# Kernel optimization log

Hardware: AMD Instinct MI355X
Metric: run time of the kernel (lower is better)

The kernel has to match this reference:

```python
import jax, jax.numpy as jnp
import numpy as np

ANCHOR_SIZES = (128.0, 256.0, 512.0)
ANCHOR_RATIOS = (0.5, 1.0, 2.0)
IOU_THR = 0.3


def _conv(x, w, b, pad):
    y = jax.lax.conv_general_dilated(
        x, w, window_strides=(1, 1), padding=[(pad, pad), (pad, pad)],
        dimension_numbers=("NCHW", "OIHW", "NCHW"))
    return y + b[None, :, None, None]


def _make_anchors(grid_h, grid_w, stride):
    # torchvision-style cell anchors (ratio-major over scales), rounded
    scales = jnp.asarray(ANCHOR_SIZES, jnp.float32)
    ratios = jnp.asarray(ANCHOR_RATIOS, jnp.float32)
    h_r = jnp.sqrt(ratios)
    w_r = 1.0 / h_r
    ws = (w_r[:, None] * scales[None, :]).reshape(-1)  # (A,)
    hs = (h_r[:, None] * scales[None, :]).reshape(-1)
    base = jnp.round(jnp.stack([-ws, -hs, ws, hs], axis=1) / 2.0)  # (A,4)
    sx = jnp.arange(grid_w, dtype=jnp.float32) * stride
    sy = jnp.arange(grid_h, dtype=jnp.float32) * stride
    yy, xx = jnp.meshgrid(sy, sx, indexing="ij")
    shifts = jnp.stack([xx, yy, xx, yy], axis=-1).reshape(-1, 4)  # (HW,4)
    return (shifts[:, None, :] + base[None, :, :]).reshape(-1, 4)  # (HW*A,4)


def _apply_box(anchors, deltas):
    w = anchors[:, 2] - anchors[:, 0]
    h = anchors[:, 3] - anchors[:, 1]
    cx = anchors[:, 0] + 0.5 * w
    cy = anchors[:, 1] + 0.5 * h
    pcx = deltas[:, 0] * w + cx
    pcy = deltas[:, 1] * h + cy
    pw = jnp.exp(deltas[:, 2]) * w
    ph = jnp.exp(deltas[:, 3]) * h
    return jnp.stack([pcx - 0.5 * pw, pcy - 0.5 * ph,
                      pcx + 0.5 * pw, pcy + 0.5 * ph], axis=1)


def _clip(boxes, img_h, img_w):
    x1 = jnp.clip(boxes[:, 0], 0.0, img_w)
    y1 = jnp.clip(boxes[:, 1], 0.0, img_h)
    x2 = jnp.clip(boxes[:, 2], 0.0, img_w)
    y2 = jnp.clip(boxes[:, 3], 0.0, img_h)
    return jnp.stack([x1, y1, x2, y2], axis=1)


def _nms_keep(boxes, scores, thr):
    # returns boolean keep mask in ORIGINAL box order (all idxs identical in
    # the source's batched_nms call, so this is plain NMS)
    n = boxes.shape[0]
    order = jnp.argsort(-scores)
    b = boxes[order]
    area = (b[:, 2] - b[:, 0]) * (b[:, 3] - b[:, 1])
    lt = jnp.maximum(b[:, None, :2], b[None, :, :2])
    rb = jnp.minimum(b[:, None, 2:], b[None, :, 2:])
    wh = jnp.clip(rb - lt, 0.0, None)
    inter = wh[..., 0] * wh[..., 1]
    iou = inter / (area[:, None] + area[None, :] - inter + 1e-9)  # (N,N)
    idx = jnp.arange(n)

    def body(i, keep):
        sup = (iou[i] > thr) & (idx > i)
        return jnp.where(keep[i], keep & ~sup, keep)

    keep_sorted = jax.lax.fori_loop(0, n, body, jnp.ones(n, bool))
    return jnp.zeros(n, bool).at[order].set(keep_sorted)


def setup_inputs() -> dict:
    key = jax.random.key(0)
    ks = jax.random.split(key, 7)
    C, H, W = 256, 32, 32
    A = len(ANCHOR_SIZES) * len(ANCHOR_RATIOS)  # 9
    return {
        "features": jax.random.normal(ks[0], (1, C, H, W), jnp.float32),
        "image_size": 512,
        "conv_w": jax.random.normal(ks[1], (512, C, 3, 3), jnp.float32) * 0.01,
        "conv_b": jnp.zeros((512,), jnp.float32),
        "cls_w": jax.random.normal(ks[2], (2 * A, 512, 1, 1), jnp.float32) * 0.01,
        "cls_b": jnp.zeros((2 * A,), jnp.float32),
        "bbox_w": jax.random.normal(ks[3], (4 * A, 512, 1, 1), jnp.float32) * 0.01,
        "bbox_b": jnp.zeros((4 * A,), jnp.float32),
    }


def reference(features, image_size, conv_w, conv_b, cls_w, cls_b, bbox_w, bbox_b):
    img_h = img_w = float(image_size)
    x = jax.nn.relu(_conv(features, conv_w, conv_b, pad=1))
    logits = _conv(x, cls_w, cls_b, pad=0)          # (1, 2A, H, W)
    bbox_pred = _conv(x, bbox_w, bbox_b, pad=0)     # (1, 4A, H, W)
    probs = jax.nn.sigmoid(logits)
    fg_scores = probs[:, 1::2, :, :].reshape(-1)    # same flatten order as torch
    grid_h, grid_w = features.shape[2], features.shape[3]
    stride = image_size // grid_h
    anchors = _make_anchors(grid_h, grid_w, float(stride))
    proposals = _apply_box(anchors, bbox_pred.reshape(-1, 4))
    proposals = _clip(proposals, img_h, img_w)
    keep = _nms_keep(proposals, fg_scores, IOU_THR)
    # fixed-shape output: suppressed boxes zeroed, plus the keep mask
    return proposals * keep[:, None].astype(proposals.dtype), probs, keep
```

## Files before the change

kernel.cpp:

```cpp
#include <hip/hip_runtime.h>
#include <math.h>

#define X_B      0
#define BBOX_B   2097152
#define PROPS_B  2244608
#define KEYS_B   2392064
#define RANK_B   2465792
#define SKEYS_B  2502656
#define SBOX_B   2576384
#define MASK_B   2725888
#define WS_NEED  13400000

typedef unsigned long long u64;
typedef double v4d __attribute__((ext_vector_type(4)));

__global__ __launch_bounds__(256, 2) void conv3x3_mfma_k(
    const float* __restrict__ feat, const float* __restrict__ w,
    const float* __restrict__ bias, float* __restrict__ xout)
{
  __shared__ float wl[9280];
  __shared__ float fl[8768];

  const int tid = threadIdx.x;
  const int bid = blockIdx.x;
  const int ct = ((bid & 7) << 2) | ((bid >> 3) >> 4);
  const int g  = (bid >> 3) & 15;
  const int co0 = ct << 4;
  const int y0  = g << 1;

  for (int i = tid; i < 8768; i += 256) fl[i] = 0.0f;

  const int lane = tid & 63, wv = tid >> 6;
  const int q = lane >> 4, n = lane & 15;
  const int wy = wv >> 1, xb = (wv & 1) << 4;
  const int xn = xb + n;

  v4d ac0 = {0.0, 0.0, 0.0, 0.0}, ac1 = {0.0, 0.0, 0.0, 0.0};
  v4d ac2 = {0.0, 0.0, 0.0, 0.0}, ac3 = {0.0, 0.0, 0.0, 0.0};
  const float4* feat4 = (const float4*)feat;

  __syncthreads();

  for (int c = 0; c < 4; ++c) {
    const int cb = c << 6;
    #pragma unroll
    for (int i = 0; i < 9; ++i) {
      const int idx4 = tid + (i << 8);
      const int co = idx4 / 144;
      const int s4 = idx4 - co * 144;
      *(float4*)&wl[co * 580 + (s4 << 2)] =
          *(const float4*)(w + (co0 + co) * 2304 + c * 576 + (s4 << 2));
    }
    #pragma unroll
    for (int i = 0; i < 8; ++i) {
      const int idx4 = tid + (i << 8);
      const int ci = idx4 >> 5;
      const int rr = (idx4 >> 3) & 3;
      const int x4 = idx4 & 7;
      const int grow = y0 - 1 + rr;
      if ((unsigned)grow < 32u) {
        const float4 v = feat4[((cb + ci) << 8) + (grow << 3) + x4];
        float* p = &fl[ci * 137 + rr * 34 + 1 + (x4 << 2)];
        p[0] = v.x; p[1] = v.y; p[2] = v.z; p[3] = v.w;
      }
    }
    __syncthreads();
    #pragma unroll
    for (int tap = 0; tap < 9; ++tap) {
      const int ky = tap / 3, kx = tap - 3 * (tap / 3);
      const float* ab = &wl[n * 580 + q * 9 + tap];
      const float* bb = &fl[q * 137 + (wy + ky) * 34 + xn + kx];
      #pragma unroll
      for (int u = 0; u < 16; u += 4) {
        ac0 = __builtin_amdgcn_mfma_f64_16x16x4f64(
            (double)ab[(u + 0) * 36], (double)bb[(u + 0) * 548], ac0, 0, 0, 0);
        ac1 = __builtin_amdgcn_mfma_f64_16x16x4f64(
            (double)ab[(u + 1) * 36], (double)bb[(u + 1) * 548], ac1, 0, 0, 0);
        ac2 = __builtin_amdgcn_mfma_f64_16x16x4f64(
            (double)ab[(u + 2) * 36], (double)bb[(u + 2) * 548], ac2, 0, 0, 0);
        ac3 = __builtin_amdgcn_mfma_f64_16x16x4f64(
            (double)ab[(u + 3) * 36], (double)bb[(u + 3) * 548], ac3, 0, 0, 0);
      }
    }
    __syncthreads();
  }

  const int pbase = (g << 6) + (wv << 4) + n;
  #pragma unroll
  for (int i = 0; i < 4; ++i) {
    const int co = co0 + q + (i << 2);
    const double s = (ac0[i] + ac1[i]) + (ac2[i] + ac3[i]);
    const double v = fmax(s + (double)bias[co], 0.0);
    xout[(co << 10) + pbase] = (float)v;
  }
}

#define CPITCH 38
#define CCHS   (18 * CPITCH)
__global__ __launch_bounds__(256) void conv3x3_relu_fb_k(
    const float* __restrict__ feat, const float* __restrict__ w,
    const float* __restrict__ bias, float* __restrict__ xout)
{
  __shared__ float il[2][8 * CCHS];
  const int cp = blockIdx.x >> 1, h = blockIdx.x & 1;
  const int tid = threadIdx.x;
  const int h16 = h << 4;
  const int co0 = cp << 1;
  for (int i = tid; i < 8 * CCHS; i += 256) { il[0][i] = 0.0f; il[1][i] = 0.0f; }
  const int yl = tid >> 4;
  const int x0 = (tid & 15) << 1;
  double aA0 = 0.0, aA1 = 0.0, aB0 = 0.0, aB1 = 0.0;
  const float4* feat4 = (const float4*)feat;
  float4 pf[5]; int pch[5], pt[5], pc4[5], pok[5];
  #pragma unroll
  for (int k = 0; k < 5; ++k) {
    const int i = tid + (k << 8);
    const int ch = i / 144, rem = i - ch * 144;
    const int t = rem >> 3, c4 = rem & 7;
    const int g = h16 - 1 + t;
    pch[k] = ch; pt[k] = t; pc4[k] = c4;
    pok[k] = (i < 1152) && ((unsigned)g < 32u);
    pf[k] = pok[k] ? feat4[(ch << 8) + (g << 3) + c4] : float4{0.f,0.f,0.f,0.f};
  }
  __syncthreads();
  for (int cc = 0; cc < 256; cc += 8) {
    const int buf = (cc >> 3) & 1;
    #pragma unroll
    for (int k = 0; k < 5; ++k)
      if (pok[k]) {
        float* p = &il[buf][pch[k] * CCHS + pt[k] * CPITCH + (pc4[k] << 2) + 1];
        p[0] = pf[k].x; p[1] = pf[k].y; p[2] = pf[k].z; p[3] = pf[k].w;
      }
    if (cc + 8 < 256) {
      #pragma unroll
      for (int k = 0; k < 5; ++k) {
        const int g = h16 - 1 + pt[k];
        if (pok[k]) pf[k] = feat4[((cc + 8 + pch[k]) << 8) + (g << 3) + pc4[k]];
      }
    }
    __syncthreads();
    #pragma unroll
    for (int cl = 0; cl < 8; ++cl) {
      const float* wAp = w + co0 * 2304 + (cc + cl) * 9;
      const float* wBp = wAp + 2304;
      double wa[9], wb[9];
      #pragma unroll
      for (int q = 0; q < 9; ++q) { wa[q] = (double)wAp[q]; wb[q] = (double)wBp[q]; }
      const float* ir = &il[buf][cl * CCHS + yl * CPITCH + x0];
      #pragma unroll
      for (int ky = 0; ky < 3; ++ky) {
        const float2 q0 = *(const float2*)(ir + ky * CPITCH);
        const float2 q1 = *(const float2*)(ir + ky * CPITCH + 2);
        const double v0 = (double)q0.x, v1 = (double)q0.y;
        const double v2 = (double)q1.x, v3 = (double)q1.y;
        aA0 += v0 * wa[3*ky+0] + v1 * wa[3*ky+1] + v2 * wa[3*ky+2];
        aA1 += v1 * wa[3*ky+0] + v2 * wa[3*ky+1] + v3 * wa[3*ky+2];
        aB0 += v0 * wb[3*ky+0] + v1 * wb[3*ky+1] + v2 * wb[3*ky+2];
        aB1 += v1 * wb[3*ky+0] + v2 * wb[3*ky+1] + v3 * wb[3*ky+2];
      }
    }
  }
  const double bA = (double)bias[co0], bB = (double)bias[co0 + 1];
  const int y = h16 + yl;
  float2 rA, rB;
  rA.x = (float)fmax(aA0 + bA, 0.0); rA.y = (float)fmax(aA1 + bA, 0.0);
  rB.x = (float)fmax(aB0 + bB, 0.0); rB.y = (float)fmax(aB1 + bB, 0.0);
  *(float2*)&xout[(co0 << 10) + (y << 5) + x0] = rA;
  *(float2*)&xout[((co0 + 1) << 10) + (y << 5) + x0] = rB;
}

__global__ __launch_bounds__(256) void head1x1_k(
    const float* __restrict__ x,
    const float* __restrict__ cls_w, const float* __restrict__ cls_b,
    const float* __restrict__ bbox_w, const float* __restrict__ bbox_b,
    float* __restrict__ out, float* __restrict__ bbox_out)
{
  __shared__ float wl[512];
  const int bid = blockIdx.x;
  const int co = bid >> 2;
  const int px = ((bid & 3) << 8) | threadIdx.x;
  const bool is_cls = co < 18;
  const float* wsrc = is_cls ? (cls_w + co * 512) : (bbox_w + (co - 18) * 512);
  for (int i = threadIdx.x; i < 512; i += 256) wl[i] = wsrc[i];
  __syncthreads();
  double acc0 = 0.0, acc1 = 0.0, acc2 = 0.0, acc3 = 0.0;
  #pragma unroll 4
  for (int c = 0; c < 512; c += 4) {
    acc0 += (double)x[((c + 0) << 10) | px] * (double)wl[c + 0];
    acc1 += (double)x[((c + 1) << 10) | px] * (double)wl[c + 1];
    acc2 += (double)x[((c + 2) << 10) | px] * (double)wl[c + 2];
    acc3 += (double)x[((c + 3) << 10) | px] * (double)wl[c + 3];
  }
  double acc = ((acc0 + acc1) + (acc2 + acc3)) +
               (double)(is_cls ? cls_b[co] : bbox_b[co - 18]);
  if (is_cls)
    out[36864 + (co << 10) + px] = (float)(1.0 / (1.0 + exp(-acc)));
  else
    bbox_out[((co - 18) << 10) + px] = (float)acc;
}

__global__ __launch_bounds__(256) void proposals_k(
    const float* __restrict__ bbox, const int* __restrict__ imgsz,
    const float* __restrict__ out, float* __restrict__ props,
    u64* __restrict__ keys, unsigned* __restrict__ rank)
{
  const int r = blockIdx.x * 256 + threadIdx.x;
  if (r >= 9216) return;
  const float4 d = ((const float4*)bbox)[r];
  const int cell = r / 9, a = r - cell * 9;
  const int ix = cell & 31, iy = cell >> 5;
  const int ri = a / 3, si = a - ri * 3;
  const double ratio = (ri == 0) ? 0.5 : (ri == 1 ? 1.0 : 2.0);
  const double scale = (si == 0) ? 128.0 : (si == 1 ? 256.0 : 512.0);
  const double hr = sqrt(ratio), wr = 1.0 / hr;
  const double bx = nearbyint(wr * scale * 0.5);
  const double by = nearbyint(hr * scale * 0.5);
  const double cx = ix * 16.0, cy = iy * 16.0;
  const double w = 2.0 * bx, hh = 2.0 * by;
  const double pcx = (double)d.x * w + cx;
  const double pcy = (double)d.y * hh + cy;
  const double pw = exp((double)d.z) * w;
  const double ph = exp((double)d.w) * hh;
  const double im = (double)imgsz[0];
  float4 o;
  o.x = (float)fmin(fmax(pcx - 0.5 * pw, 0.0), im);
  o.y = (float)fmin(fmax(pcy - 0.5 * ph, 0.0), im);
  o.z = (float)fmin(fmax(pcx + 0.5 * pw, 0.0), im);
  o.w = (float)fmin(fmax(pcy + 0.5 * ph, 0.0), im);
  ((float4*)props)[r] = o;
  const float s = out[36864 + ((2 * (r >> 10) + 1) << 10) + (r & 1023)];
  keys[r] = ((u64)__float_as_uint(s) << 32) | (unsigned)(0x7FFFFFFF - r);
  rank[r] = 0u;
}

__global__ __launch_bounds__(256) void rank_k(
    const u64* __restrict__ keys, unsigned* __restrict__ rank)
{
  const int jt = blockIdx.x % 36, ic = blockIdx.x / 36;
  const int j = jt * 256 + threadIdx.x;
  const u64 kj = keys[j];
  const int lane = threadIdx.x & 63;
  const int base = ic * 576;
  unsigned lo[9], hi[9];
  #pragma unroll
  for (int rr = 0; rr < 9; ++rr) {
    const u64 k = keys[base + rr * 64 + lane];
    lo[rr] = (unsigned)k; hi[rr] = (unsigned)(k >> 32);
  }
  unsigned cnt = 0;
  #pragma unroll
  for (int rr = 0; rr < 9; ++rr) {
    #pragma unroll
    for (int l = 0; l < 64; ++l) {
      const unsigned llo = (unsigned)__builtin_amdgcn_readlane((int)lo[rr], l);
      const unsigned lhi = (unsigned)__builtin_amdgcn_readlane((int)hi[rr], l);
      const u64 ki = ((u64)lhi << 32) | llo;
      cnt += (ki > kj) ? 1u : 0u;
    }
  }
  atomicAdd(&rank[j], cnt);
}

__global__ __launch_bounds__(256) void scatter_k(
    const u64* __restrict__ keys, const unsigned* __restrict__ rank,
    const float* __restrict__ props, u64* __restrict__ skeys,
    float4* __restrict__ sboxes)
{
  const int r = blockIdx.x * 256 + threadIdx.x;
  if (r >= 9216) return;
  const unsigned rk = rank[r];
  skeys[rk] = keys[r];
  sboxes[rk] = ((const float4*)props)[r];
}

__global__ __launch_bounds__(256) void mask_k(
    const float4* __restrict__ sb4, u64* __restrict__ mask)
{
  __shared__ __align__(16) float4 ib[64];
  const int ci = blockIdx.x;
  const int Wb = blockIdx.y << 2;
  const int i_lo = ci << 6;
  const int i_hi = min(i_lo + 64, (Wb + 4) << 6);
  if (i_lo >= i_hi) return;
  const int wv = threadIdx.x >> 6, lane = threadIdx.x & 63;
  const int W = Wb + wv;
  const int cnt = i_hi - i_lo;
  if (threadIdx.x < cnt) ib[threadIdx.x] = sb4[i_lo + threadIdx.x];
  __syncthreads();
  const float4 bj = sb4[(W << 6) + lane];
  const float areaJ = (bj.z - bj.x) * (bj.w - bj.y);
  const int n = i_hi - i_lo;
  #pragma unroll 8
  for (int k = 0; k < n; ++k) {
    const float4 bi = ib[k];
    const float areaI = (bi.z - bi.x) * (bi.w - bi.y);
    const float ix1 = fmaxf(bj.x, bi.x), iy1 = fmaxf(bj.y, bi.y);
    const float ix2 = fminf(bj.z, bi.z), iy2 = fminf(bj.w, bi.w);
    const float iw = fmaxf(ix2 - ix1, 0.0f), ih = fmaxf(iy2 - iy1, 0.0f);
    const double inter = (double)iw * (double)ih;
    const double uni = (double)areaJ + (double)areaI - inter + 1e-9;
    const bool pred = inter > 0.3 * uni;
    const u64 bal = __ballot(pred);
    const int i = i_lo + k;
    if (lane == 0) mask[(size_t)i * 144 + W] = bal;
  }
}

__global__ __launch_bounds__(1024) void sweep_out_k(
    const u64* __restrict__ mask, const u64* __restrict__ skeys,
    const float4* __restrict__ sboxes, float* __restrict__ out)
{
  extern __shared__ __align__(16) char sm[];
  u64* subm   = (u64*)sm;
  u64* supS   = subm + 9216;
  u64* keptS  = supS + 16;
  unsigned short* kpl = (unsigned short*)(keptS + 144);
  int* kcnt  = (int*)(kpl + 9216);
  int* kprev = kcnt + 1;

  const int tid = threadIdx.x;
  const int lane = tid & 63, wv = tid >> 6;
  if (tid == 0) { *kcnt = 0; *kprev = 0; }
  if (tid < 144) keptS[tid] = 0ULL;
  if (tid < 16) supS[tid] = 0ULL;
  if (tid < 512) {
    const int wq = tid & 7, r0 = tid >> 3;
    #pragma unroll
    for (int k = 0; k < 8; ++k) {
      const int i = r0 + (k << 6);
      subm[i * 9 + wq] = mask[(size_t)i * 144 + wq];
    }
  }
  __syncthreads();

  for (int sg = 0; sg < 18; ++sg) {
    const int buf = sg & 1, nb = buf ^ 1;
    const int wbase = sg << 3;
    const int ibase = wbase << 6;
    const int P = *kprev, K = *kcnt;
    if (K > P) {
      const int wq = tid & 7, str = tid >> 3;
      u64 acc = 0ULL;
      for (int j = P + str; j < K; j += 128)
        acc |= mask[(size_t)kpl[j] * 144 + wbase + wq];
      if (acc) {
        atomicOr((unsigned*)&supS[(buf << 3) + wq], (unsigned)acc);
        atomicOr(((unsigned*)&supS[(buf << 3) + wq]) + 1, (unsigned)(acc >> 32));
      }
    }
    if (tid >= 1008) ((unsigned*)&supS[nb << 3])[tid - 1008] = 0u;
    __syncthreads();
    if (wv == 0) {
      u64 myAlive = (lane < 8) ? ~supS[(buf << 3) + lane] : 0ULL;
      const u64* sub = subm + buf * 4608;
      u64 rowL8[8];
      #pragma unroll
      for (int w = 0; w < 8; ++w)
        rowL8[w] = sub[((w << 6) + lane) * 9 + w];
      #pragma unroll
      for (int w = 0; w < 8; ++w) {
        const u64 av = __shfl(myAlive, w, 64);
        if (av == 0ULL) continue;
        const u64 rowL = rowL8[w];
        u64 cand = av, keptw = 0ULL;
        while (cand) {
          const int b = (int)__builtin_ctzll(cand);
          keptw |= 1ULL << b;
          const u64 sup =
              ((u64)(unsigned)__builtin_amdgcn_readlane((int)(rowL >> 32), b)
               << 32) |
              (unsigned)__builtin_amdgcn_readlane((int)rowL, b);
          cand &= ~(sup | (1ULL << b));
        }
        if (lane == 0) keptS[wbase + w] = keptw;
        if (keptw) {
          const int K2 = *kcnt;
          if ((keptw >> lane) & 1ULL) {
            const int pre =
                __builtin_popcountll(keptw & ((1ULL << lane) - 1ULL));
            kpl[K2 + pre] = (unsigned short)(ibase + (w << 6) + lane);
          }
          if (lane == 0) *kcnt = K2 + __builtin_popcountll(keptw);
          u64 t = keptw;
          while (t) {
            int bs[8]; int nn = 0;
            #pragma unroll
            for (int s = 0; s < 8; ++s) {
              if (t) { bs[s] = (int)__builtin_ctzll(t); t &= t - 1ULL; nn = s + 1; }
              else bs[s] = 0;
            }
            const int kk = lane >> 3, wq = lane & 7;
            u64 r = (kk < nn) ? sub[((w << 6) + bs[kk]) * 9 + wq] : 0ULL;
            r |= __shfl_down(r, 8, 64);
            r |= __shfl_down(r, 16, 64);
            r |= __shfl_down(r, 32, 64);
            myAlive &= ~r;
          }
        }
      }
    } else if (wv == 1) {
      if (lane == 0) *kprev = K;
    } else if (wv < 8) {
      if (sg + 1 < 18 && K > 0) {
        const int t6 = tid - 128;
        const int wq = t6 & 7, str = t6 >> 3;
        const int wb2 = (sg + 1) << 3;
        u64 acc = 0ULL;
        int j = str;
        for (; j + 3 * 48 < K; j += 4 * 48) {
          const u64 a0 = mask[(size_t)kpl[j + 0 * 48] * 144 + wb2 + wq];
          const u64 a1 = mask[(size_t)kpl[j + 1 * 48] * 144 + wb2 + wq];
          const u64 a2 = mask[(size_t)kpl[j + 2 * 48] * 144 + wb2 + wq];
          const u64 a3 = mask[(size_t)kpl[j + 3 * 48] * 144 + wb2 + wq];
          acc |= (a0 | a1) | (a2 | a3);
        }
        for (; j < K; j += 48)
          acc |= mask[(size_t)kpl[j] * 144 + wb2 + wq];
        if (acc) {
          atomicOr((unsigned*)&supS[(nb << 3) + wq], (unsigned)acc);
          atomicOr(((unsigned*)&supS[(nb << 3) + wq]) + 1, (unsigned)(acc >> 32));
        }
      }
    } else if (sg + 1 < 18) {
      const int s = tid - 512;
      const int wq = s & 7, r0 = s >> 3;
      const int ib2 = (sg + 1) << 9;
      const int wb2 = (sg + 1) << 3;
      #pragma unroll
      for (int k = 0; k < 8; ++k) {
        const int i = r0 + (k << 6);
        subm[nb * 4608 + i * 9 + wq] = mask[(size_t)(ib2 + i) * 144 + wb2 + wq];
      }
    }
    __syncthreads();
  }
  for (int i = tid; i < 9216; i += 1024) {
    const u64 key = skeys[i];
    const int orig = 0x7FFFFFFF - (int)(unsigned)(key & 0xFFFFFFFFULL);
    const bool kp = (keptS[i >> 6] >> (i & 63)) & 1ULL;
    float4 ob = sboxes[i];
    if (!kp) { ob.x = 0.f; ob.y = 0.f; ob.z = 0.f; ob.w = 0.f; }
    ((float4*)out)[orig] = ob;
    out[55296 + orig] = kp ? 1.0f : 0.0f;
  }
}

__global__ __launch_bounds__(1024) void nms_fallback_k(
    const float* __restrict__ props, float* __restrict__ out)
{
  __shared__ u64 wmax[16];
  __shared__ float4 curBoxS;
  const int tid = threadIdx.x, wid = tid >> 6, lane = tid & 63;
  u64 key[9];
  float4 box[9];
  #pragma unroll
  for (int j = 0; j < 9; ++j) {
    const int r = tid + (j << 10);
    box[j] = ((const float4*)props)[r];
    const float s = out[36864 + ((2 * (r >> 10) + 1) << 10) + (r & 1023)];
    key[j] = ((u64)__float_as_uint(s) << 32) | (unsigned)(0x7FFFFFFF - r);
  }
  unsigned kept = 0;
  for (;;) {
    u64 m = key[0];
    #pragma unroll
    for (int j = 1; j < 9; ++j) m = key[j] > m ? key[j] : m;
    #pragma unroll
    for (int off = 32; off; off >>= 1) {
      const u64 o = __shfl_down(m, off, 64);
      if (o > m) m = o;
    }
    if (lane == 0) wmax[wid] = m;
    __syncthreads();
    u64 K = wmax[0];
    #pragma unroll
    for (int wv2 = 1; wv2 < 16; ++wv2) { const u64 t = wmax[wv2]; if (t > K) K = t; }
    if (K == 0) break;
    #pragma unroll
    for (int j = 0; j < 9; ++j)
      if (key[j] == K) { curBoxS = box[j]; key[j] = 0; kept |= 1u << j; }
    __syncthreads();
    const float4 cb = curBoxS;
    const float areaC = (cb.z - cb.x) * (cb.w - cb.y);
    #pragma unroll
    for (int j = 0; j < 9; ++j) {
      if (key[j]) {
        const float4 b = box[j];
        const float ix1 = fmaxf(b.x, cb.x), iy1 = fmaxf(b.y, cb.y);
        const float ix2 = fminf(b.z, cb.z), iy2 = fminf(b.w, cb.w);
        const float iw = fmaxf(ix2 - ix1, 0.0f), ih = fmaxf(iy2 - iy1, 0.0f);
        const float areaB = (b.z - b.x) * (b.w - b.y);
        const double inter = (double)iw * (double)ih;
        const double uni = (double)areaB + (double)areaC - inter + 1e-9;
        if (inter > 0.3 * uni) key[j] = 0;
      }
    }
    __syncthreads();
  }
  #pragma unroll
  for (int j = 0; j < 9; ++j) {
    const int r = tid + (j << 10);
    const bool kp = (kept >> j) & 1u;
    float4 ob = box[j];
    if (!kp) { ob.x = 0.f; ob.y = 0.f; ob.z = 0.f; ob.w = 0.f; }
    ((float4*)out)[r] = ob;
    out[55296 + r] = kp ? 1.0f : 0.0f;
  }
}

extern "C" void kernel_launch(void* const* d_in, const int* in_sizes, int n_in,
                              void* d_out, int out_size, void* d_ws, size_t ws_size,
                              hipStream_t stream)
{
  const float* feat   = (const float*)d_in[0];
  const int*   imgsz  = (const int*)d_in[1];
  const float* conv_w = (const float*)d_in[2];
  const float* conv_b = (const float*)d_in[3];
  const float* cls_w  = (const float*)d_in[4];
  const float* cls_b  = (const float*)d_in[5];
  const float* bbox_w = (const float*)d_in[6];
  const float* bbox_b = (const float*)d_in[7];
  float* out = (float*)d_out;
  char*  ws  = (char*)d_ws;
  float* x      = (float*)(ws + X_B);
  float* bbox   = (float*)(ws + BBOX_B);
  float* props  = (float*)(ws + PROPS_B);
  u64*      keys  = (u64*)(ws + KEYS_B);
  unsigned* rankp = (unsigned*)(ws + RANK_B);
  u64*      skeys = (u64*)(ws + SKEYS_B);
  float4*   sboxs = (float4*)(ws + SBOX_B);
  u64*      maskp = (u64*)(ws + MASK_B);

  if (ws_size >= (size_t)WS_NEED) {
    hipLaunchKernelGGL(conv3x3_mfma_k, dim3(512), dim3(256), 0, stream,
                       feat, conv_w, conv_b, x);
    hipLaunchKernelGGL(head1x1_k, dim3(216), dim3(256), 0, stream,
                       x, cls_w, cls_b, bbox_w, bbox_b, out, bbox);
    hipLaunchKernelGGL(proposals_k, dim3(36), dim3(256), 0, stream,
                       bbox, imgsz, out, props, keys, rankp);
    hipLaunchKernelGGL(rank_k, dim3(576), dim3(256), 0, stream, keys, rankp);
    hipLaunchKernelGGL(scatter_k, dim3(36), dim3(256), 0, stream,
                       keys, rankp, props, skeys, sboxs);
    hipLaunchKernelGGL(mask_k, dim3(144, 36), dim3(256), 0, stream,
                       sboxs, maskp);
    hipLaunchKernelGGL(sweep_out_k, dim3(1), dim3(1024), 93448, stream,
                       maskp, skeys, sboxs, out);
  } else {
    hipLaunchKernelGGL(conv3x3_relu_fb_k, dim3(512), dim3(256), 0, stream,
                       feat, conv_w, conv_b, x);
    hipLaunchKernelGGL(head1x1_k, dim3(216), dim3(256), 0, stream,
                       x, cls_w, cls_b, bbox_w, bbox_b, out, bbox);
    hipLaunchKernelGGL(proposals_k, dim3(36), dim3(256), 0, stream,
                       bbox, imgsz, out, props, keys, rankp);
    hipLaunchKernelGGL(nms_fallback_k, dim3(1), dim3(1024), 0, stream,
                       props, out);
  }
}
```

Before: 251.3 us.

## Remove one barrier per NMS sweep group by folding delta suppression into wave 0

Measured after the change: 249.7 us. Within noise of the previous version (-0.7%).

```diff
diff --git a/kernel.cpp b/kernel.cpp
--- a/kernel.cpp
+++ b/kernel.cpp
@@ -316,11 +316,10 @@
   u64* keptS  = supS + 16;
   unsigned short* kpl = (unsigned short*)(keptS + 144);
   int* kcnt  = (int*)(kpl + 9216);
-  int* kprev = kcnt + 1;
 
   const int tid = threadIdx.x;
   const int lane = tid & 63, wv = tid >> 6;
-  if (tid == 0) { *kcnt = 0; *kprev = 0; }
+  if (tid == 0) *kcnt = 0;
   if (tid < 144) keptS[tid] = 0ULL;
   if (tid < 16) supS[tid] = 0ULL;
   if (tid < 512) {
@@ -333,30 +332,38 @@
   }
   __syncthreads();
 
+  int Kpp = 0, Kp = 0;
+
   for (int sg = 0; sg < 18; ++sg) {
     const int buf = sg & 1, nb = buf ^ 1;
     const int wbase = sg << 3;
     const int ibase = wbase << 6;
-    const int P = *kprev, K = *kcnt;
-    if (K > P) {
-      const int wq = tid & 7, str = tid >> 3;
-      u64 acc = 0ULL;
-      for (int j = P + str; j < K; j += 128)
-        acc |= mask[(size_t)kpl[j] * 144 + wbase + wq];
-      if (acc) {
-        atomicOr((unsigned*)&supS[(buf << 3) + wq], (unsigned)acc);
-        atomicOr(((unsigned*)&supS[(buf << 3) + wq]) + 1, (unsigned)(acc >> 32));
-      }
-    }
-    if (tid >= 1008) ((unsigned*)&supS[nb << 3])[tid - 1008] = 0u;
-    __syncthreads();
     if (wv == 0) {
-      u64 myAlive = (lane < 8) ? ~supS[(buf << 3) + lane] : 0ULL;
+      u64 dacc = 0ULL;
+      {
+        const int wq = lane & 7;
+        int j = Kpp + (lane >> 3);
+        for (; j + 24 < Kp; j += 32) {
+          const u64 a0 = mask[(size_t)kpl[j +  0] * 144 + wbase + wq];
+          const u64 a1 = mask[(size_t)kpl[j +  8] * 144 + wbase + wq];
+          const u64 a2 = mask[(size_t)kpl[j + 16] * 144 + wbase + wq];
+          const u64 a3 = mask[(size_t)kpl[j + 24] * 144 + wbase + wq];
+          dacc |= (a0 | a1) | (a2 | a3);
+        }
+        for (; j < Kp; j += 8)
+          dacc |= mask[(size_t)kpl[j] * 144 + wbase + wq];
+      }
+      dacc |= __shfl_xor(dacc, 8, 64);
+      dacc |= __shfl_xor(dacc, 16, 64);
+      dacc |= __shfl_xor(dacc, 32, 64);
+      u64 myAlive = (lane < 8) ? ~(supS[(buf << 3) + lane] | dacc) : 0ULL;
+      if (lane < 8) supS[(buf << 3) + lane] = 0ULL;
       const u64* sub = subm + buf * 4608;
       u64 rowL8[8];
       #pragma unroll
       for (int w = 0; w < 8; ++w)
         rowL8[w] = sub[((w << 6) + lane) * 9 + w];
+      int Kcur = Kp;
       #pragma unroll
       for (int w = 0; w < 8; ++w) {
         const u64 av = __shfl(myAlive, w, 64);
@@ -374,13 +381,12 @@
         }
         if (lane == 0) keptS[wbase + w] = keptw;
         if (keptw) {
-          const int K2 = *kcnt;
           if ((keptw >> lane) & 1ULL) {
             const int pre =
                 __builtin_popcountll(keptw & ((1ULL << lane) - 1ULL));
-            kpl[K2 + pre] = (unsigned short)(ibase + (w << 6) + lane);
+            kpl[Kcur + pre] = (unsigned short)(ibase + (w << 6) + lane);
           }
-          if (lane == 0) *kcnt = K2 + __builtin_popcountll(keptw);
+          Kcur += __builtin_popcountll(keptw);
           u64 t = keptw;
           while (t) {
             int bs[8]; int nn = 0;
@@ -398,23 +404,24 @@
           }
         }
       }
-    } else if (wv == 1) {
-      if (lane == 0) *kprev = K;
-    } else if (wv < 8) {
-      if (sg + 1 < 18 && K > 0) {
-        const int t6 = tid - 128;
+      Kpp = Kp; Kp = Kcur;
+      if (lane == 0) *kcnt = Kcur;
+    } else if (wv < 12) {
+      if (sg + 1 < 18) {
+        const int Kh = *kcnt;
+        const int t6 = tid - 64;
         const int wq = t6 & 7, str = t6 >> 3;
         const int wb2 = (sg + 1) << 3;
         u64 acc = 0ULL;
         int j = str;
-        for (; j + 3 * 48 < K; j += 4 * 48) {
-          const u64 a0 = mask[(size_t)kpl[j + 0 * 48] * 144 + wb2 + wq];
-          const u64 a1 = mask[(size_t)kpl[j + 1 * 48] * 144 + wb2 + wq];
-          const u64 a2 = mask[(size_t)kpl[j + 2 * 48] * 144 + wb2 + wq];
-          const u64 a3 = mask[(size_t)kpl[j + 3 * 48] * 144 + wb2 + wq];
+        for (; j + 3 * 88 < Kh; j += 4 * 88) {
+          const u64 a0 = mask[(size_t)kpl[j + 0 * 88] * 144 + wb2 + wq];
+          const u64 a1 = mask[(size_t)kpl[j + 1 * 88] * 144 + wb2 + wq];
+          const u64 a2 = mask[(size_t)kpl[j + 2 * 88] * 144 + wb2 + wq];
+          const u64 a3 = mask[(size_t)kpl[j + 3 * 88] * 144 + wb2 + wq];
           acc |= (a0 | a1) | (a2 | a3);
         }
-        for (; j < K; j += 48)
+        for (; j < Kh; j += 88)
           acc |= mask[(size_t)kpl[j] * 144 + wb2 + wq];
         if (acc) {
           atomicOr((unsigned*)&supS[(nb << 3) + wq], (unsigned)acc);
@@ -422,13 +429,13 @@
         }
       }
     } else if (sg + 1 < 18) {
-      const int s = tid - 512;
+      const int s = tid - 768;
       const int wq = s & 7, r0 = s >> 3;
       const int ib2 = (sg + 1) << 9;
       const int wb2 = (sg + 1) << 3;
       #pragma unroll
-      for (int k = 0; k < 8; ++k) {
-        const int i = r0 + (k << 6);
+      for (int k = 0; k < 16; ++k) {
+        const int i = r0 + (k << 5);
         subm[nb * 4608 + i * 9 + wq] = mask[(size_t)(ib2 + i) * 144 + wb2 + wq];
       }
     }
@@ -543,7 +550,7 @@
                        keys, rankp, props, skeys, sboxs);
     hipLaunchKernelGGL(mask_k, dim3(144, 36), dim3(256), 0, stream,
                        sboxs, maskp);
-    hipLaunchKernelGGL(sweep_out_k, dim3(1), dim3(1024), 93448, stream,
+    hipLaunchKernelGGL(sweep_out_k, dim3(1), dim3(1024), 93444, stream,
                        maskp, skeys, sboxs, out);
   } else {
     hipLaunchKernelGGL(conv3x3_relu_fb_k, dim3(512), dim3(256), 0, stream,
```
